# Optimization experiments

Measured on AMD Instinct MI355X. Metric: run time of the kernel, lower is better.

Reference implementation:

```python
import jax, jax.numpy as jnp
import numpy as np

BIOSYNTHETIC_FAMILIES = {'glutamate': ['E','Q','P','R','K'], 'aspartate': ['D','N','T','I','M','K'], 'serine': ['S','G','C'], 'pyruvate': ['A','V','L'], 'aromatic': ['F','Y','W'], 'histidine': ['H']}
CODON_TABLE = {'UUU':'F','UUC':'F','UUA':'L','UUG':'L','CUU':'L','CUC':'L','CUA':'L','CUG':'L','AUU':'I','AUC':'I','AUA':'I','AUG':'M','GUU':'V','GUC':'V','GUA':'V','GUG':'V','UCU':'S','UCC':'S','UCA':'S','UCG':'S','CCU':'P','CCC':'P','CCA':'P','CCG':'P','ACU':'T','ACC':'T','ACA':'T','ACG':'T','GCU':'A','GCC':'A','GCA':'A','GCG':'A','UAU':'Y','UAC':'Y','UAA':'*','UAG':'*','CAU':'H','CAC':'H','CAA':'Q','CAG':'Q','AAU':'N','AAC':'N','AAA':'K','AAG':'K','GAU':'D','GAC':'D','GAA':'E','GAG':'E','UGU':'C','UGC':'C','UGA':'*','UGG':'W','CGU':'R','CGC':'R','CGA':'R','CGG':'R','AGU':'S','AGC':'S','AGA':'R','AGG':'R','GGU':'G','GGC':'G','GGA':'G','GGG':'G'}

def _build_family_matrix():
    aa2fam = {aa: f for f, aas in BIOSYNTHETIC_FAMILIES.items() for aa in aas}
    codons = list(CODON_TABLE.keys())
    fam = [aa2fam.get(CODON_TABLE[c]) for c in codons]  # None for stop codons
    M = np.zeros((64, 64), dtype=np.float32)
    for i in range(64):
        for j in range(64):
            if fam[i] is not None and fam[j] is not None and fam[i] == fam[j]:
                M[i, j] = 1.0
    return jnp.asarray(M)

FAMILY_MATRIX = _build_family_matrix()  # (64, 64) constant lookup table

def setup_inputs() -> dict:
    key = jax.random.key(0)
    k1, k2 = jax.random.split(key)
    codon_embeddings = jax.random.normal(k1, (16, 512, 16), dtype=jnp.float32)
    codon_indices = jax.random.randint(k2, (16, 512), 0, 64, dtype=jnp.int64 if jax.config.jax_enable_x64 else jnp.int32)
    return {"codon_embeddings": codon_embeddings, "codon_indices": codon_indices}

def reference(codon_embeddings, codon_indices):
    b, s, d = codon_embeddings.shape
    emb = codon_embeddings.reshape(-1, d)            # (n, d)
    idx = codon_indices.reshape(-1)                  # (n,)
    # Euclidean pairwise distances (torch.cdist, p=2)
    sq = jnp.sum(emb * emb, axis=-1)                 # (n,)
    d2 = sq[:, None] + sq[None, :] - 2.0 * (emb @ emb.T)
    d2 = jnp.maximum(d2, 0.0)
    mask = d2 > 0.0
    dist = jnp.where(mask, jnp.sqrt(jnp.where(mask, d2, 1.0)), 0.0)  # (n, n)
    # Same-family mask via 64x64 lookup gather
    same = FAMILY_MATRIX[idx[:, None], idx[None, :]]  # (n, n)
    eps = 1e-10
    same_sum = jnp.sum(same)
    total = jnp.asarray(dist.shape[0] * dist.shape[1], dist.dtype)
    same_d = jnp.sum(dist * same) / (same_sum + eps)
    diff_d = (jnp.sum(dist) - jnp.sum(dist * same)) / ((total - same_sum) + eps)
    loss = same_d - 0.5 * diff_d + 1.0
    return jax.nn.relu(loss)
```

## Files before the change

kernel.cpp:

```cpp
#include <hip/hip_runtime.h>
#include <math.h>

#define N_ROWS 8192
#define D 16
#define TILE 128
#define NT 64
#define NBLK 2080

#define OFF_PT   0
#define OFF_PS   16384

typedef short  bf16x8 __attribute__((ext_vector_type(8)));
typedef float  f32x4  __attribute__((ext_vector_type(4)));

#if __has_builtin(__builtin_amdgcn_sqrtf)
#define SQRTF(x) __builtin_amdgcn_sqrtf(x)
#else
#define SQRTF(x) sqrtf(x)
#endif

__device__ __constant__ signed char FAM_LUT[64] = {
  4,4,3,3, 3,3,3,3,
  1,1,1,1, 3,3,3,3,
  2,2,2,2, 0,0,0,0,
  1,1,1,1, 3,3,3,3,
  4,4,-1,-1, 5,5,0,0,
  1,1,1,1, 1,1,0,0,
  2,2,-1,4, 0,0,0,0,
  2,2,0,0, 2,2,2,2
};

__device__ __forceinline__ unsigned short f2bf(float f) {
  unsigned u = __float_as_uint(f);
  u += 0x7fffu + ((u >> 16) & 1u);
  return (unsigned short)(u >> 16);
}
__device__ __forceinline__ float bf2f(unsigned short s) {
  return __uint_as_float((unsigned)s << 16);
}

__global__ __launch_bounds__(512, 4) void pair_kernel(
    const float* __restrict__ emb, const int* __restrict__ idx,
    float* __restrict__ pt, float* __restrict__ ps) {
  const int u = blockIdx.y, bx = blockIdx.x;
  int it, jt;
  if (bx < NT - u) { it = u;          jt = u + bx; }
  else             { it = NT - 1 - u; jt = bx - 1; }

  __shared__ __align__(16) unsigned short BH[2048];
  __shared__ __align__(16) unsigned short BL[2048];
  __shared__ float2 SFJ[TILE];
  __shared__ float  SQI[TILE];
  __shared__ float  FAI[TILE];
  __shared__ float  rT[8], rS[8];

  const int t  = threadIdx.x;
  const int w  = t >> 6;
  const int l  = t & 63;
  const int lr = l & 15;
  const int g  = l >> 4;
  const int half = g & 1;

  if (t < 256) {
    const int local = t & 127;
    const int row = ((t < 128) ? it : jt) * TILE + local;
    const float4* s4 = (const float4*)(emb + (size_t)row * D);
    float4 a0 = s4[0], a1 = s4[1], a2 = s4[2], a3 = s4[3];
    float v[16];
    v[0]=a0.x; v[1]=a0.y; v[2]=a0.z; v[3]=a0.w;
    v[4]=a1.x; v[5]=a1.y; v[6]=a1.z; v[7]=a1.w;
    v[8]=a2.x; v[9]=a2.y; v[10]=a2.z; v[11]=a2.w;
    v[12]=a3.x; v[13]=a3.y; v[14]=a3.z; v[15]=a3.w;
    float ss = v[0] * v[0];
#pragma unroll
    for (int k = 1; k < 16; ++k) ss = fmaf(v[k], v[k], ss);
    const int f = FAM_LUT[idx[row] & 63];
    if (t < 128) { SQI[local] = ss; FAI[local] = (f >= 0) ? (float)f : -1.0f; }
    else         { SFJ[local] = make_float2(ss, (f >= 0) ? (float)f : -2.0f); }
  }

  if (t < 256) {
    const int mjs = t >> 5, hs = (t >> 4) & 1, lrs = t & 15;
    const int row = jt * TILE + mjs * 16 + lrs;
    const float4* s4 = (const float4*)(emb + (size_t)row * D + hs * 8);
    float4 b0 = s4[0], b1 = s4[1];
    float vb[8];
    vb[0]=b0.x; vb[1]=b0.y; vb[2]=b0.z; vb[3]=b0.w;
    vb[4]=b1.x; vb[5]=b1.y; vb[6]=b1.z; vb[7]=b1.w;
    unsigned short h8[8], l8[8];
#pragma unroll
    for (int k = 0; k < 8; ++k) {
      h8[k] = f2bf(vb[k]);
      l8[k] = f2bf(vb[k] - bf2f(h8[k]));
    }
    *(bf16x8*)(BH + t * 8) = *(bf16x8*)h8;
    *(bf16x8*)(BL + t * 8) = *(bf16x8*)l8;
  }

  const int arow = it * TILE + w * 16 + lr;
  const float4* a4 = (const float4*)(emb + (size_t)arow * D + half * 8);
  float4 c0 = a4[0], c1 = a4[1];
  float va[8];
  va[0]=c0.x; va[1]=c0.y; va[2]=c0.z; va[3]=c0.w;
  va[4]=c1.x; va[5]=c1.y; va[6]=c1.z; va[7]=c1.w;
  unsigned short f8[8];
#pragma unroll
  for (int k = 0; k < 8; ++k) {
    const unsigned short h = f2bf(va[k]);
    f8[k] = (g < 2) ? h : f2bf(va[k] - bf2f(h));
  }
  const bf16x8 afrag = *(bf16x8*)f8;

  __syncthreads();

  float sqi[4], fai[4];
#pragma unroll
  for (int r = 0; r < 4; ++r) {
    sqi[r] = SQI[w * 16 + g * 4 + r];
    fai[r] = FAI[w * 16 + g * 4 + r];
  }

  const int bofs = (half * 16 + lr) * 8;
  float accT = 0.0f, accS = 0.0f;
#pragma unroll 2
  for (int mj = 0; mj < 8; ++mj) {
    const bf16x8 bhi = *(const bf16x8*)(BH + mj * 256 + bofs);
    const bf16x8 blo = *(const bf16x8*)(BL + mj * 256 + bofs);
    const float2 sfj = SFJ[mj * 16 + lr];
    f32x4 acc = {0.0f, 0.0f, 0.0f, 0.0f};
    acc = __builtin_amdgcn_mfma_f32_16x16x32_bf16(afrag, blo, acc, 0, 0, 0);
    acc = __builtin_amdgcn_mfma_f32_16x16x32_bf16(afrag, bhi, acc, 0, 0, 0);
#pragma unroll
    for (int r = 0; r < 4; ++r) {
      float d2 = fmaf(-2.0f, acc[r], sqi[r] + sfj.x);
      d2 = fmaxf(d2, 0.0f);
      const float dist = SQRTF(d2);
      accT += dist;
      accS += (fai[r] == sfj.y) ? dist : 0.0f;
    }
  }

#pragma unroll
  for (int off = 32; off > 0; off >>= 1) {
    accT += __shfl_down(accT, off);
    accS += __shfl_down(accS, off);
  }
  if (l == 0) { rT[w] = accT; rS[w] = accS; }
  __syncthreads();
  if (t == 0) {
    float sT = 0.0f, sS = 0.0f;
#pragma unroll
    for (int k = 0; k < 8; ++k) { sT += rT[k]; sS += rS[k]; }
    const float wgt = (it == jt) ? 1.0f : 2.0f;
    const int bid = blockIdx.y * gridDim.x + blockIdx.x;
    pt[bid] = wgt * sT;
    ps[bid] = wgt * sS;
  }
}

__global__ __launch_bounds__(512) void final_kernel(
    const float* __restrict__ pt, const float* __restrict__ ps,
    const int* __restrict__ idx, float* __restrict__ out) {
  const int t = threadIdx.x, w = t >> 6, l = t & 63;
  __shared__ float  HW[8][8];
  __shared__ double rTd[8], rSd[8];

  float myCnt = 0.0f;
#pragma unroll
  for (int rr = 0; rr < 16; ++rr) {
    const int f = FAM_LUT[idx[rr * 512 + t] & 63];
#pragma unroll
    for (int fam = 0; fam < 6; ++fam) {
      const unsigned long long m = __ballot(f == fam);
      if (l == fam) myCnt += (float)__popcll(m);
    }
  }
  if (l < 8) HW[w][l] = (l < 6) ? myCnt : 0.0f;

  double sT = 0.0, sS = 0.0;
  for (int k = t; k < NBLK; k += 512) { sT += (double)pt[k]; sS += (double)ps[k]; }
#pragma unroll
  for (int off = 32; off > 0; off >>= 1) {
    sT += __shfl_down(sT, off);
    sS += __shfl_down(sS, off);
  }
  if (l == 0) { rTd[w] = sT; rSd[w] = sS; }
  __syncthreads();
  if (t == 0) {
    double tot = 0.0, sam = 0.0;
#pragma unroll
    for (int k = 0; k < 8; ++k) { tot += rTd[k]; sam += rSd[k]; }
    double same_sum = 0.0;
    for (int f = 0; f < 6; ++f) {
      double c = 0.0;
      for (int k = 0; k < 8; ++k) c += (double)HW[k][f];
      same_sum += c * c;
    }
    const double total  = (double)N_ROWS * (double)N_ROWS;
    const double same_d = sam / (same_sum + 1e-10);
    const double diff_d = (tot - sam) / (total - same_sum + 1e-10);
    double loss = same_d - 0.5 * diff_d + 1.0;
    out[0] = (float)(loss > 0.0 ? loss : 0.0);
  }
}

extern "C" void kernel_launch(void* const* d_in, const int* in_sizes, int n_in,
                              void* d_out, int out_size, void* d_ws, size_t ws_size,
                              hipStream_t stream) {
  const float* emb = (const float*)d_in[0];
  const int*   idx = (const int*)d_in[1];
  char* ws = (char*)d_ws;
  float* pt = (float*)(ws + OFF_PT);
  float* ps = (float*)(ws + OFF_PS);

  pair_kernel<<<dim3(NT + 1, NT / 2), dim3(512), 0, stream>>>(emb, idx, pt, ps);
  final_kernel<<<dim3(1), dim3(512), 0, stream>>>(pt, ps, idx, (float*)d_out);
}
```

Measured before the change: 27.02 us.

## Process two column tiles per block with triangular pair indexing

Each block now handles one row tile against two adjacent column tiles, so the grid over the upper triangle shrinks from 2080 blocks to 1056. The block index is mapped to (it, jt0) with a closed-form triangular inversion, and padding tiles past the edge are masked out with zero weights. The -2 scale is folded into the A fragment and the squared norms into the MFMA accumulator init, which removes per-element FMAs. This halves per-block launch and row-tile setup overhead and reuses the A fragment across twice the work, at the cost of more shared memory, more registers per thread and some wasted compute on edge tiles.

```diff
diff --git a/kernel.cpp b/kernel.cpp
--- a/kernel.cpp
+++ b/kernel.cpp
@@ -5,10 +5,10 @@
 #define D 16
 #define TILE 128
 #define NT 64
-#define NBLK 2080
+#define NPAIR 1056
 
 #define OFF_PT   0
-#define OFF_PS   16384
+#define OFF_PS   8192
 
 typedef short  bf16x8 __attribute__((ext_vector_type(8)));
 typedef float  f32x4  __attribute__((ext_vector_type(4)));
@@ -38,18 +38,29 @@
 __device__ __forceinline__ float bf2f(unsigned short s) {
   return __uint_as_float((unsigned)s << 16);
 }
+__device__ __forceinline__ int S_of(int m) {
+  return (m & 1) ? (((m + 1) * (m + 1)) >> 2) : ((m * (m + 2)) >> 2);
+}
 
 __global__ __launch_bounds__(512, 4) void pair_kernel(
     const float* __restrict__ emb, const int* __restrict__ idx,
     float* __restrict__ pt, float* __restrict__ ps) {
-  const int u = blockIdx.y, bx = blockIdx.x;
-  int it, jt;
-  if (bx < NT - u) { it = u;          jt = u + bx; }
-  else             { it = NT - 1 - u; jt = bx - 1; }
-
-  __shared__ __align__(16) unsigned short BH[2048];
-  __shared__ __align__(16) unsigned short BL[2048];
-  __shared__ float2 SFJ[TILE];
+  const int b = blockIdx.x;
+  const int cc = NPAIR - b;
+  int m = (int)(2.0f * sqrtf((float)cc));
+  if (m > NT) m = NT;
+  if (m < 1) m = 1;
+  while (S_of(m) < cc) ++m;
+  while (m > 1 && S_of(m - 1) >= cc) --m;
+  const int it  = NT - m;
+  const int p   = b - (NPAIR - S_of(m));
+  const int jt0 = it + 2 * p;
+  const int jt1 = jt0 + 1;
+  const bool v1 = (jt1 < NT);
+
+  __shared__ __align__(16) unsigned short BH[4096];
+  __shared__ __align__(16) unsigned short BL[4096];
+  __shared__ float2 SFJ[256];
   __shared__ float  SQI[TILE];
   __shared__ float  FAI[TILE];
   __shared__ float  rT[8], rS[8];
@@ -61,9 +72,17 @@
   const int g  = l >> 4;
   const int half = g & 1;
 
-  if (t < 256) {
-    const int local = t & 127;
-    const int row = ((t < 128) ? it : jt) * TILE + local;
+  if (t < 384) {
+    const bool iside = (t < 128);
+    const int  local = iside ? t : (t - 128);
+    bool valid = true;
+    int row;
+    if (iside) row = it * TILE + local;
+    else {
+      const int jtile = (local < 128) ? jt0 : jt1;
+      valid = (jtile < NT);
+      row = min(jtile, NT - 1) * TILE + (local & 127);
+    }
     const float4* s4 = (const float4*)(emb + (size_t)row * D);
     float4 a0 = s4[0], a1 = s4[1], a2 = s4[2], a3 = s4[3];
     float v[16];
@@ -75,13 +94,19 @@
 #pragma unroll
     for (int k = 1; k < 16; ++k) ss = fmaf(v[k], v[k], ss);
     const int f = FAM_LUT[idx[row] & 63];
-    if (t < 128) { SQI[local] = ss; FAI[local] = (f >= 0) ? (float)f : -1.0f; }
-    else         { SFJ[local] = make_float2(ss, (f >= 0) ? (float)f : -2.0f); }
-  }
-
-  if (t < 256) {
-    const int mjs = t >> 5, hs = (t >> 4) & 1, lrs = t & 15;
-    const int row = jt * TILE + mjs * 16 + lrs;
+    if (iside) { SQI[local] = ss; FAI[local] = (f >= 0) ? (float)f : -1.0f; }
+    else {
+      SFJ[local] = make_float2(valid ? ss : 0.0f,
+                               valid ? ((f >= 0) ? (float)f : -2.0f) : -3.0f);
+    }
+  }
+
+  {
+    const int ti = t >> 8, c8 = t & 255;
+    const int mjs = c8 >> 5, hs = (c8 >> 4) & 1, lrs = c8 & 15;
+    const int jtile = ti ? jt1 : jt0;
+    const bool valid = (jtile < NT);
+    const int row = min(jtile, NT - 1) * TILE + mjs * 16 + lrs;
     const float4* s4 = (const float4*)(emb + (size_t)row * D + hs * 8);
     float4 b0 = s4[0], b1 = s4[1];
     float vb[8];
@@ -90,8 +115,9 @@
     unsigned short h8[8], l8[8];
 #pragma unroll
     for (int k = 0; k < 8; ++k) {
-      h8[k] = f2bf(vb[k]);
-      l8[k] = f2bf(vb[k] - bf2f(h8[k]));
+      const unsigned short h = f2bf(vb[k]);
+      h8[k] = valid ? h : (unsigned short)0;
+      l8[k] = valid ? f2bf(vb[k] - bf2f(h)) : (unsigned short)0;
     }
     *(bf16x8*)(BH + t * 8) = *(bf16x8*)h8;
     *(bf16x8*)(BL + t * 8) = *(bf16x8*)l8;
@@ -106,8 +132,9 @@
   unsigned short f8[8];
 #pragma unroll
   for (int k = 0; k < 8; ++k) {
-    const unsigned short h = f2bf(va[k]);
-    f8[k] = (g < 2) ? h : f2bf(va[k] - bf2f(h));
+    const float sv = -2.0f * va[k];
+    const unsigned short h = f2bf(sv);
+    f8[k] = (g < 2) ? h : f2bf(sv - bf2f(h));
   }
   const bf16x8 afrag = *(bf16x8*)f8;
 
@@ -121,25 +148,30 @@
   }
 
   const int bofs = (half * 16 + lr) * 8;
-  float accT = 0.0f, accS = 0.0f;
-#pragma unroll 2
-  for (int mj = 0; mj < 8; ++mj) {
-    const bf16x8 bhi = *(const bf16x8*)(BH + mj * 256 + bofs);
-    const bf16x8 blo = *(const bf16x8*)(BL + mj * 256 + bofs);
+  float tT0 = 0.0f, tS0 = 0.0f, tT1 = 0.0f, tS1 = 0.0f;
+#pragma unroll
+  for (int mj = 0; mj < 16; ++mj) {
+    const int base = (mj >> 3) * 2048 + (mj & 7) * 256 + bofs;
+    const bf16x8 bhi = *(const bf16x8*)(BH + base);
+    const bf16x8 blo = *(const bf16x8*)(BL + base);
     const float2 sfj = SFJ[mj * 16 + lr];
-    f32x4 acc = {0.0f, 0.0f, 0.0f, 0.0f};
+    f32x4 acc = { sqi[0] + sfj.x, sqi[1] + sfj.x, sqi[2] + sfj.x, sqi[3] + sfj.x };
     acc = __builtin_amdgcn_mfma_f32_16x16x32_bf16(afrag, blo, acc, 0, 0, 0);
     acc = __builtin_amdgcn_mfma_f32_16x16x32_bf16(afrag, bhi, acc, 0, 0, 0);
 #pragma unroll
     for (int r = 0; r < 4; ++r) {
-      float d2 = fmaf(-2.0f, acc[r], sqi[r] + sfj.x);
-      d2 = fmaxf(d2, 0.0f);
+      const float d2   = fmaxf(acc[r], 0.0f);
       const float dist = SQRTF(d2);
-      accT += dist;
-      accS += (fai[r] == sfj.y) ? dist : 0.0f;
-    }
-  }
-
+      const float sm   = (fai[r] == sfj.y) ? dist : 0.0f;
+      if (mj < 8) { tT0 += dist; tS0 += sm; }
+      else        { tT1 += dist; tS1 += sm; }
+    }
+  }
+
+  const float w0 = (jt0 == it) ? 1.0f : 2.0f;
+  const float w1 = v1 ? 2.0f : 0.0f;
+  float accT = fmaf(w0, tT0, w1 * tT1);
+  float accS = fmaf(w0, tS0, w1 * tS1);
 #pragma unroll
   for (int off = 32; off > 0; off >>= 1) {
     accT += __shfl_down(accT, off);
@@ -151,10 +183,8 @@
     float sT = 0.0f, sS = 0.0f;
 #pragma unroll
     for (int k = 0; k < 8; ++k) { sT += rT[k]; sS += rS[k]; }
-    const float wgt = (it == jt) ? 1.0f : 2.0f;
-    const int bid = blockIdx.y * gridDim.x + blockIdx.x;
-    pt[bid] = wgt * sT;
-    ps[bid] = wgt * sS;
+    pt[b] = sT;
+    ps[b] = sS;
   }
 }
 
@@ -171,14 +201,14 @@
     const int f = FAM_LUT[idx[rr * 512 + t] & 63];
 #pragma unroll
     for (int fam = 0; fam < 6; ++fam) {
-      const unsigned long long m = __ballot(f == fam);
-      if (l == fam) myCnt += (float)__popcll(m);
+      const unsigned long long mk = __ballot(f == fam);
+      if (l == fam) myCnt += (float)__popcll(mk);
     }
   }
   if (l < 8) HW[w][l] = (l < 6) ? myCnt : 0.0f;
 
   double sT = 0.0, sS = 0.0;
-  for (int k = t; k < NBLK; k += 512) { sT += (double)pt[k]; sS += (double)ps[k]; }
+  for (int k = t; k < NPAIR; k += 512) { sT += (double)pt[k]; sS += (double)ps[k]; }
 #pragma unroll
   for (int off = 32; off > 0; off >>= 1) {
     sT += __shfl_down(sT, off);
@@ -213,6 +243,6 @@
   float* pt = (float*)(ws + OFF_PT);
   float* ps = (float*)(ws + OFF_PS);
 
-  pair_kernel<<<dim3(NT + 1, NT / 2), dim3(512), 0, stream>>>(emb, idx, pt, ps);
+  pair_kernel<<<dim3(NPAIR), dim3(512), 0, stream>>>(emb, idx, pt, ps);
   final_kernel<<<dim3(1), dim3(512), 0, stream>>>(pt, ps, idx, (float*)d_out);
 }
```

New measurement: 27.46 us. Within noise of the previous version (+1.6%).
